# Kernel optimization log

Measured on AMD Instinct MI355X. Metric: run time of the kernel, lower is better.

Reference implementation:

```python
import jax, jax.numpy as jnp
import numpy as np

NEG_SLOPE = 0.2
N_GRAPHS = 32

def gat_conv(x, src, dst, W, attn_l, attn_r, bias):
    """DGL-style GATConv: returns [N, H, D]."""
    H, D = attn_l.shape
    N = x.shape[0]
    feat = (x @ W).reshape(N, H, D)                     # [N,H,D]
    el = jnp.sum(feat * attn_l[None], axis=-1)          # [N,H]
    er = jnp.sum(feat * attn_r[None], axis=-1)          # [N,H]
    e = jax.nn.leaky_relu(el[src] + er[dst], NEG_SLOPE) # [E,H]
    # edge softmax over incoming edges of each dst node
    emax = jax.ops.segment_max(e, dst, num_segments=N)
    emax = jnp.where(jnp.isfinite(emax), emax, 0.0)     # zero in-degree guard
    ex = jnp.exp(e - emax[dst])
    den = jax.ops.segment_sum(ex, dst, num_segments=N)
    alpha = ex / jnp.maximum(den[dst], 1e-9)            # [E,H]
    msg = alpha[:, :, None] * feat[src]                 # [E,H,D]
    rst = jax.ops.segment_sum(msg, dst, num_segments=N) # [N,H,D]
    return rst + bias.reshape(1, H, D)

def branch(x, src, dst, gid, W1, al1, ar1, b1, W2, al2, ar2, b2):
    h = jax.nn.relu(gat_conv(x, src, dst, W1, al1, ar1, b1))  # [N,10,64]
    h = h.sum(axis=1)                                          # [N,64]
    h = jax.nn.relu(gat_conv(h, src, dst, W2, al2, ar2, b2))  # [N,1,128]
    h = h[:, 0, :]                                             # [N,128]
    g = jax.ops.segment_max(h, gid, num_segments=N_GRAPHS)     # [B,128] max readout
    return jnp.where(jnp.isfinite(g), g, 0.0)

def reference(lig_x, lig_src, lig_dst, lig_gid, rec_x, rec_src, rec_dst, rec_gid,
              W1l, al1l, ar1l, b1l, W2l, al2l, ar2l, b2l,
              W1r, al1r, ar1r, b1r, W2r, al2r, ar2r, b2r,
              Wlin1, blin1, Wlin2, blin2):
    hlig = branch(lig_x, lig_src, lig_dst, lig_gid, W1l, al1l, ar1l, b1l, W2l, al2l, ar2l, b2l)
    hrec = branch(rec_x, rec_src, rec_dst, rec_gid, W1r, al1r, ar1r, b1r, W2r, al2r, ar2r, b2r)
    h = jnp.concatenate([hlig, hrec], axis=1)           # [B,256]
    h = jax.nn.relu(h @ Wlin1 + blin1)
    h = jax.nn.relu(h @ Wlin2 + blin2)
    return h.reshape(-1)

def setup_inputs() -> dict:
    key = jax.random.key(0)
    ks = jax.random.split(key, 24)
    Nl, El, Nr, Er = 20000, 160000, 40000, 400000
    d = {}
    d['lig_x'] = jax.random.normal(ks[0], (Nl, 64), jnp.float32)
    d['lig_src'] = jax.random.randint(ks[1], (El,), 0, Nl, jnp.int32)
    d['lig_dst'] = jax.random.randint(ks[2], (El,), 0, Nl, jnp.int32)
    d['lig_gid'] = jnp.sort(jax.random.randint(ks[3], (Nl,), 0, N_GRAPHS, jnp.int32))
    d['rec_x'] = jax.random.normal(ks[4], (Nr, 64), jnp.float32)
    d['rec_src'] = jax.random.randint(ks[5], (Er,), 0, Nr, jnp.int32)
    d['rec_dst'] = jax.random.randint(ks[6], (Er,), 0, Nr, jnp.int32)
    d['rec_gid'] = jnp.sort(jax.random.randint(ks[7], (Nr,), 0, N_GRAPHS, jnp.int32))
    s = 0.1
    d['W1l'] = jax.random.normal(ks[8], (64, 640), jnp.float32) * s
    d['al1l'] = jax.random.normal(ks[9], (10, 64), jnp.float32) * s
    d['ar1l'] = jax.random.normal(ks[10], (10, 64), jnp.float32) * s
    d['b1l'] = jnp.zeros((640,), jnp.float32)
    d['W2l'] = jax.random.normal(ks[11], (64, 128), jnp.float32) * s
    d['al2l'] = jax.random.normal(ks[12], (1, 128), jnp.float32) * s
    d['ar2l'] = jax.random.normal(ks[13], (1, 128), jnp.float32) * s
    d['b2l'] = jnp.zeros((128,), jnp.float32)
    d['W1r'] = jax.random.normal(ks[14], (64, 640), jnp.float32) * s
    d['al1r'] = jax.random.normal(ks[15], (10, 64), jnp.float32) * s
    d['ar1r'] = jax.random.normal(ks[16], (10, 64), jnp.float32) * s
    d['b1r'] = jnp.zeros((640,), jnp.float32)
    d['W2r'] = jax.random.normal(ks[17], (64, 128), jnp.float32) * s
    d['al2r'] = jax.random.normal(ks[18], (1, 128), jnp.float32) * s
    d['ar2r'] = jax.random.normal(ks[19], (1, 128), jnp.float32) * s
    d['b2r'] = jnp.zeros((128,), jnp.float32)
    d['Wlin1'] = jax.random.normal(ks[20], (256, 128), jnp.float32) * s
    d['blin1'] = jnp.zeros((128,), jnp.float32)
    d['Wlin2'] = jax.random.normal(ks[21], (128, 1), jnp.float32) * s
    d['blin2'] = jnp.zeros((1,), jnp.float32)
    return d
```

## Files before the change

### kernel.cpp

```cpp
#include <hip/hip_runtime.h>
#include <hip/hip_bf16.h>

typedef short bf16x8 __attribute__((ext_vector_type(8)));
typedef float f32x4 __attribute__((ext_vector_type(4)));

__device__ inline float lrelu(float x) { return x > 0.f ? x : 0.2f * x; }

__device__ inline unsigned short f2bf(float f) {
    unsigned u = __float_as_uint(f);
    u = u + 0x7FFFu + ((u >> 16) & 1u);
    return (unsigned short)(u >> 16);
}

__global__ void copy_x2(const float4* __restrict__ a, int na4,
                        const float4* __restrict__ b, int nb4, float4* __restrict__ o) {
    int total = na4 + nb4;
    int stride = gridDim.x * blockDim.x;
    for (int i = blockIdx.x * blockDim.x + threadIdx.x; i < total; i += stride)
        o[i] = (i < na4) ? a[i] : b[i - na4];
}

__global__ void fold_attn(const float* __restrict__ W, const float* __restrict__ al,
                          const float* __restrict__ ar, float* __restrict__ Walr,
                          int H, int D) {
    int k = blockIdx.x;
    int lane = threadIdx.x;
    int C = H * D;
    for (int h = 0; h < H; ++h) {
        float sl = 0.f, sr = 0.f;
        for (int d = lane; d < D; d += 64) {
            float w = W[(size_t)k * C + h * D + d];
            sl += w * al[h * D + d];
            sr += w * ar[h * D + d];
        }
        for (int off = 32; off; off >>= 1) {
            sl += __shfl_down(sl, off);
            sr += __shfl_down(sr, off);
        }
        if (lane == 0) {
            Walr[k * 2 * H + h] = sl;
            Walr[k * 2 * H + H + h] = sr;
        }
    }
}

__global__ void prep_walr(const float* __restrict__ Walr, unsigned short* __restrict__ F,
                          int C2) {
    int NCT = (C2 + 15) / 16;
    int total = NCT * 1024;
    int stride = gridDim.x * blockDim.x;
    for (int idx = blockIdx.x * blockDim.x + threadIdx.x; idx < total; idx += stride) {
        int j = idx & 7;
        int lane = (idx >> 3) & 63;
        int step = (idx >> 9) & 1;
        int CT = idx >> 10;
        int k = ((lane >> 4) << 3) + j + (step << 5);
        int col = (CT << 4) + (lane & 15);
        F[idx] = (col < C2) ? f2bf(Walr[k * C2 + col]) : 0;
    }
}

template <int H>
__global__ __launch_bounds__(256) void attn_mfma(const float* __restrict__ x,
                                                 const bf16x8* __restrict__ Wf,
                                                 float* __restrict__ el,
                                                 float* __restrict__ er, int N) {
    const int NCT = (2 * H + 15) / 16;
    int lane = threadIdx.x & 63;
    int w = threadIdx.x >> 6;
    int row0 = blockIdx.x * 64 + w * 16;
    int arow = row0 + (lane & 15);
    if (arow > N - 1) arow = N - 1;
    int kb = (lane >> 4) * 8;
    int colL = lane & 15;

    const float* xr = x + (size_t)arow * 64 + kb;
    float4 a0 = *reinterpret_cast<const float4*>(xr);
    float4 a1 = *reinterpret_cast<const float4*>(xr + 4);
    float4 a2 = *reinterpret_cast<const float4*>(xr + 32);
    float4 a3 = *reinterpret_cast<const float4*>(xr + 36);
    bf16x8 A0, A1;
    A0[0] = (short)f2bf(a0.x); A0[1] = (short)f2bf(a0.y);
    A0[2] = (short)f2bf(a0.z); A0[3] = (short)f2bf(a0.w);
    A0[4] = (short)f2bf(a1.x); A0[5] = (short)f2bf(a1.y);
    A0[6] = (short)f2bf(a1.z); A0[7] = (short)f2bf(a1.w);
    A1[0] = (short)f2bf(a2.x); A1[1] = (short)f2bf(a2.y);
    A1[2] = (short)f2bf(a2.z); A1[3] = (short)f2bf(a2.w);
    A1[4] = (short)f2bf(a3.x); A1[5] = (short)f2bf(a3.y);
    A1[6] = (short)f2bf(a3.z); A1[7] = (short)f2bf(a3.w);

    int rbase = row0 + (lane >> 4) * 4;
#pragma unroll
    for (int ct = 0; ct < NCT; ++ct) {
        bf16x8 B0 = Wf[(ct * 2 + 0) * 64 + lane];
        bf16x8 B1 = Wf[(ct * 2 + 1) * 64 + lane];
        f32x4 acc = {0, 0, 0, 0};
        acc = __builtin_amdgcn_mfma_f32_16x16x32_bf16(A0, B0, acc, 0, 0, 0);
        acc = __builtin_amdgcn_mfma_f32_16x16x32_bf16(A1, B1, acc, 0, 0, 0);
        int col = ct * 16 + colL;
#pragma unroll
        for (int r = 0; r < 4; ++r) {
            int row = rbase + r;
            if (row < N) {
                if (col < H) el[(size_t)row * H + col] = acc[r];
                else if (col < 2 * H) er[(size_t)row * H + col - H] = acc[r];
            }
        }
    }
}

__global__ void count_deg2(const int* __restrict__ dl, const int* __restrict__ dr,
                           int* __restrict__ deg, int El, int Er, int Nl) {
    int total = El + Er;
    int stride = gridDim.x * blockDim.x;
    for (int i = blockIdx.x * blockDim.x + threadIdx.x; i < total; i += stride) {
        int d = (i < El) ? dl[i] : (dr[i - El] + Nl);
        atomicAdd(&deg[d], 1);
    }
}

__global__ __launch_bounds__(256) void scan_local(const int* __restrict__ deg,
                                                  int* __restrict__ rowptr,
                                                  int* __restrict__ bsum, int N) {
    __shared__ int wsum[4];
    int t = threadIdx.x;
    int base = blockIdx.x * 2048 + t * 8;
    int v[8];
    int s = 0;
#pragma unroll
    for (int i = 0; i < 8; ++i) {
        int idx = base + i;
        v[i] = (idx < N) ? deg[idx] : 0;
        s += v[i];
    }
    int lane = t & 63, w = t >> 6;
    int incl = s;
    for (int off = 1; off < 64; off <<= 1) {
        int o = __shfl_up(incl, off);
        if (lane >= off) incl += o;
    }
    if (lane == 63) wsum[w] = incl;
    __syncthreads();
    int woff = 0;
    for (int i = 0; i < w; ++i) woff += wsum[i];
    int run = woff + incl - s;
#pragma unroll
    for (int i = 0; i < 8; ++i) {
        int idx = base + i;
        if (idx < N) rowptr[idx] = run;
        run += v[i];
    }
    if (t == 255) bsum[blockIdx.x] = woff + incl;
}

__global__ void scan_bsum(int* __restrict__ bsum, int* __restrict__ rowptrN, int nb) {
    int t = threadIdx.x;
    int v = (t < nb) ? bsum[t] : 0;
    int incl = v;
    for (int off = 1; off < 64; off <<= 1) {
        int o = __shfl_up(incl, off);
        if (t >= off) incl += o;
    }
    if (t < nb) bsum[t] = incl - v;
    if (t == 63) *rowptrN = incl;
}

__global__ __launch_bounds__(256) void scan_add(int* __restrict__ rowptr,
                                                const int* __restrict__ bsum, int N) {
    int off = bsum[blockIdx.x];
    if (off == 0) return;
    int base = blockIdx.x * 2048 + threadIdx.x * 8;
#pragma unroll
    for (int i = 0; i < 8; ++i) {
        int idx = base + i;
        if (idx < N) rowptr[idx] += off;
    }
}

__global__ void fill_adj2(const int* __restrict__ sl, const int* __restrict__ dl,
                          const int* __restrict__ sr, const int* __restrict__ dr,
                          int* __restrict__ cursor, int* __restrict__ adj,
                          int El, int Er, int Nl) {
    int total = El + Er;
    int stride = gridDim.x * blockDim.x;
    for (int i = blockIdx.x * blockDim.x + threadIdx.x; i < total; i += stride) {
        int s, d;
        if (i < El) { s = sl[i]; d = dl[i]; }
        else        { s = sr[i - El] + Nl; d = dr[i - El] + Nl; }
        int pos = atomicAdd(&cursor[d], 1);
        adj[pos] = s;
    }
}

__global__ __launch_bounds__(256) void dslot_expand(const int* __restrict__ rowptr,
                                                    int* __restrict__ dslot, int N) {
    int stride = gridDim.x * blockDim.x;
    for (int n = blockIdx.x * blockDim.x + threadIdx.x; n < N; n += stride) {
        int rb = rowptr[n], re = rowptr[n + 1];
        for (int j = rb; j < re; ++j) dslot[j] = n;
    }
}

__global__ void gstart_build2(const int* __restrict__ gidL, const int* __restrict__ gidR,
                              int* __restrict__ gs, int Nl, int Nr) {
    int Nc = Nl + Nr;
    int stride = gridDim.x * blockDim.x;
    for (int n = blockIdx.x * blockDim.x + threadIdx.x; n < Nc; n += stride) {
        if (n < Nl) {
            int gcur = gidL[n];
            int gprev = (n == 0) ? -1 : gidL[n - 1];
            for (int g = gprev + 1; g <= gcur; ++g) gs[g] = n;
            if (n == Nl - 1)
                for (int g = gcur + 1; g <= 32; ++g) gs[g] = Nl;
        } else {
            int ln = n - Nl;
            int gcur = gidR[ln];
            int gprev = (ln == 0) ? -1 : gidR[ln - 1];
            for (int g = gprev + 1; g <= gcur; ++g) gs[33 + g] = n;
            if (ln == Nr - 1)
                for (int g = gcur + 1; g <= 32; ++g) gs[33 + g] = Nc;
        }
    }
}

template <int H>
__global__ void edge_e(const int* __restrict__ adj, const int* __restrict__ dslot,
                       const float* __restrict__ el, const float* __restrict__ er,
                       float* __restrict__ e, int E) {
    int stride = gridDim.x * blockDim.x;
    for (int i = blockIdx.x * blockDim.x + threadIdx.x; i < E; i += stride) {
        int s = adj[i], d = dslot[i];
        const float* els = el + (size_t)s * H;
        const float* erd = er + (size_t)d * H;
#pragma unroll
        for (int h = 0; h < H; ++h)
            e[(size_t)i * H + h] = lrelu(els[h] + erd[h]);
    }
}

template <int H>
__global__ void node_norm(const int* __restrict__ rowptr, const float* __restrict__ e,
                          float* __restrict__ alpha, int N) {
    int stride = gridDim.x * blockDim.x;
    for (int n = blockIdx.x * blockDim.x + threadIdx.x; n < N; n += stride) {
        int rbeg = rowptr[n], rend = rowptr[n + 1];
        if (rbeg == rend) continue;
        float m[H], den[H];
#pragma unroll
        for (int h = 0; h < H; ++h) { m[h] = -INFINITY; den[h] = 0.f; }
        for (int j = rbeg; j < rend; ++j) {
#pragma unroll
            for (int h = 0; h < H; ++h) {
                float ev = e[(size_t)j * H + h];
                float newm = fmaxf(m[h], ev);
                den[h] = den[h] * __expf(m[h] - newm) + __expf(ev - newm);
                m[h] = newm;
            }
        }
        float inv[H];
#pragma unroll
        for (int h = 0; h < H; ++h) inv[h] = 1.f / fmaxf(den[h], 1e-9f);
        for (int j = rbeg; j < rend; ++j) {
#pragma unroll
            for (int h = 0; h < H; ++h)
                alpha[(size_t)j * H + h] = __expf(e[(size_t)j * H + h] - m[h]) * inv[h];
        }
    }
}

template <int H>
__global__ __launch_bounds__(256, 8) void gather_z_b(
        const int* __restrict__ rowptr, const int* __restrict__ adj,
        const float* __restrict__ alpha, const float* __restrict__ x,
        unsigned short* __restrict__ z, int N) {
    int lane = threadIdx.x & 63;
    int w = threadIdx.x >> 6;
    int wpb = blockDim.x >> 6;
    int wstride = gridDim.x * wpb;
    for (int n = blockIdx.x * wpb + w; n < N; n += wstride) {
        int rbeg = __builtin_amdgcn_readfirstlane(rowptr[n]);
        int rend = __builtin_amdgcn_readfirstlane(rowptr[n + 1]);
        float acc[H];
#pragma unroll
        for (int h = 0; h < H; ++h) acc[h] = 0.f;
        for (int base = rbeg; base < rend; base += 64) {
            int cnt = rend - base; if (cnt > 64) cnt = 64;
            int sv = adj[base + ((lane < cnt) ? lane : 0)];
            int j = 0;
            for (; j + 4 <= cnt; j += 4) {
                int s0 = __shfl(sv, j);
                int s1 = __shfl(sv, j + 1);
                int s2 = __shfl(sv, j + 2);
                int s3 = __shfl(sv, j + 3);
                float x0 = x[(size_t)s0 * 64 + lane];
                float x1 = x[(size_t)s1 * 64 + lane];
                float x2 = x[(size_t)s2 * 64 + lane];
                float x3 = x[(size_t)s3 * 64 + lane];
                const float* a0 = alpha + (size_t)(base + j) * H;
                const float* a1 = a0 + H;
                const float* a2 = a1 + H;
                const float* a3 = a2 + H;
#pragma unroll
                for (int h = 0; h < H; ++h)
                    acc[h] += a0[h] * x0 + a1[h] * x1 + a2[h] * x2 + a3[h] * x3;
            }
            for (; j < cnt; ++j) {
                int s = __shfl(sv, j);
                float xv = x[(size_t)s * 64 + lane];
                const float* al = alpha + (size_t)(base + j) * H;
#pragma unroll
                for (int h = 0; h < H; ++h) acc[h] += al[h] * xv;
            }
        }
#pragma unroll
        for (int h = 0; h < H; ++h)
            z[(size_t)n * (H * 64) + h * 64 + lane] = f2bf(acc[h]);
    }
}

__global__ void prep_wfrag(const float* __restrict__ W, unsigned short* __restrict__ F,
                           int C) {
    int total = (C >> 4) * 1024;
    int stride = gridDim.x * blockDim.x;
    for (int idx = blockIdx.x * blockDim.x + threadIdx.x; idx < total; idx += stride) {
        int j = idx & 7;
        int lane = (idx >> 3) & 63;
        int step = (idx >> 9) & 1;
        int CT = idx >> 10;
        int k = ((lane >> 4) << 3) + j + (step << 5);
        int col = (CT << 4) + (lane & 15);
        F[idx] = f2bf(W[(size_t)k * C + col]);
    }
}

template <int H>
__global__ __launch_bounds__(256) void gemm_heads_mfma_b(
        const unsigned short* __restrict__ z, const bf16x8* __restrict__ Wf,
        const float* __restrict__ bias, float* __restrict__ out, int N) {
    const int SA = H * 64;
    int lane = threadIdx.x & 63;
    int w = threadIdx.x >> 6;
    int row0 = blockIdx.x * 64 + w * 16;
    int arow = row0 + (lane & 15);
    if (arow > N - 1) arow = N - 1;
    int kb = (lane >> 4) * 8;
    int colL = lane & 15;

    f32x4 o0 = {0,0,0,0}, o1 = {0,0,0,0}, o2 = {0,0,0,0}, o3 = {0,0,0,0};

    for (int h = 0; h < H; ++h) {
        const unsigned short* zr = z + (size_t)arow * SA + h * 64 + kb;
        bf16x8 A0 = *reinterpret_cast<const bf16x8*>(zr);
        bf16x8 A1 = *reinterpret_cast<const bf16x8*>(zr + 32);

        f32x4 acc0 = {0,0,0,0}, acc1 = {0,0,0,0}, acc2 = {0,0,0,0}, acc3 = {0,0,0,0};
#define CT_STEP(accv, ct)                                                            \
        {                                                                            \
            bf16x8 B0 = Wf[((h * 4 + (ct)) * 2 + 0) * 64 + lane];                    \
            bf16x8 B1 = Wf[((h * 4 + (ct)) * 2 + 1) * 64 + lane];                    \
            accv = __builtin_amdgcn_mfma_f32_16x16x32_bf16(A0, B0, accv, 0, 0, 0);   \
            accv = __builtin_amdgcn_mfma_f32_16x16x32_bf16(A1, B1, accv, 0, 0, 0);   \
        }
        CT_STEP(acc0, 0) CT_STEP(acc1, 1) CT_STEP(acc2, 2) CT_STEP(acc3, 3)
#undef CT_STEP

#define EPI(ov, accv, ct)                                                            \
        {                                                                            \
            float bv = bias[h * 64 + (ct) * 16 + colL];                              \
            ov[0] += fmaxf(accv[0] + bv, 0.f);                                       \
            ov[1] += fmaxf(accv[1] + bv, 0.f);                                       \
            ov[2] += fmaxf(accv[2] + bv, 0.f);                                       \
            ov[3] += fmaxf(accv[3] + bv, 0.f);                                       \
        }
        EPI(o0, acc0, 0) EPI(o1, acc1, 1) EPI(o2, acc2, 2) EPI(o3, acc3, 3)
#undef EPI
    }

    int rbase = row0 + (lane >> 4) * 4;
#define ST(ov, ct)                                                                   \
    {                                                                                \
        _Pragma("unroll")                                                            \
        for (int r = 0; r < 4; ++r) {                                                \
            int row = rbase + r;                                                     \
            if (row < N) out[(size_t)row * 64 + (ct) * 16 + colL] = ov[r];           \
        }                                                                            \
    }
    ST(o0, 0) ST(o1, 1) ST(o2, 2) ST(o3, 3)
#undef ST
}

__global__ __launch_bounds__(256) void gemm_relu_mfma_b(
        const unsigned short* __restrict__ z, const bf16x8* __restrict__ Wf,
        const float* __restrict__ bias, float* __restrict__ out, int N) {
    int lane = threadIdx.x & 63;
    int w = threadIdx.x >> 6;
    int row0 = blockIdx.x * 64 + w * 16;
    int arow = row0 + (lane & 15);
    if (arow > N - 1) arow = N - 1;
    int kb = (lane >> 4) * 8;
    int colL = lane & 15;

    const unsigned short* zr = z + (size_t)arow * 64 + kb;
    bf16x8 A0 = *reinterpret_cast<const bf16x8*>(zr);
    bf16x8 A1 = *reinterpret_cast<const bf16x8*>(zr + 32);

    int rbase = row0 + (lane >> 4) * 4;
#define DO_CT(ct)                                                                    \
    {                                                                                \
        bf16x8 B0 = Wf[((ct) * 2 + 0) * 64 + lane];                                  \
        bf16x8 B1 = Wf[((ct) * 2 + 1) * 64 + lane];                                  \
        f32x4 acc = {0, 0, 0, 0};                                                    \
        acc = __builtin_amdgcn_mfma_f32_16x16x32_bf16(A0, B0, acc, 0, 0, 0);         \
        acc = __builtin_amdgcn_mfma_f32_16x16x32_bf16(A1, B1, acc, 0, 0, 0);         \
        float bv = bias[(ct) * 16 + colL];                                           \
        _Pragma("unroll")                                                            \
        for (int r = 0; r < 4; ++r) {                                                \
            int row = rbase + r;                                                     \
            if (row < N)                                                             \
                out[(size_t)row * 128 + (ct) * 16 + colL] = fmaxf(acc[r] + bv, 0.f); \
        }                                                                            \
    }
    DO_CT(0) DO_CT(1) DO_CT(2) DO_CT(3) DO_CT(4) DO_CT(5) DO_CT(6) DO_CT(7)
#undef DO_CT
}

__global__ __launch_bounds__(128) void graph_max2(const float* __restrict__ rst2,
                                                  const int* __restrict__ gstart,
                                                  float* __restrict__ gm) {
    int g = blockIdx.x;
    int b = g >> 5, gl = g & 31;
    int sp = blockIdx.y;
    int t = threadIdx.x;
    const int* gs = gstart + 33 * b;
    int rb = gs[gl], re = gs[gl + 1];
    float m = -INFINITY;
    for (int r = rb + sp; r < re; r += 8)
        m = fmaxf(m, rst2[(size_t)r * 128 + t]);
    gm[(size_t)((b * 8 + sp) * 32 + gl) * 128 + t] = m;
}

__global__ __launch_bounds__(256) void mlp_head2(
        const float* __restrict__ gml, const float* __restrict__ gmr,
        const float* __restrict__ W1, const float* __restrict__ b1,
        const float* __restrict__ W2, const float* __restrict__ b2,
        float* __restrict__ out) {
    __shared__ float hcat[256];
    __shared__ float part[256];
    __shared__ float h[128];
    int g = blockIdx.x;
    int t = threadIdx.x;
    {
        const float* gsrc = (t < 128) ? gml : gmr;
        int c = t & 127;
        float m = -INFINITY;
#pragma unroll
        for (int sp = 0; sp < 8; ++sp) m = fmaxf(m, gsrc[sp * 4096 + g * 128 + c]);
        hcat[t < 128 ? c : 128 + c] = fmaxf(m, 0.f);
    }
    __syncthreads();
    {
        int c = t & 127;
        int k0 = (t >> 7) << 7;
        float acc = 0.f;
#pragma unroll 4
        for (int k = 0; k < 128; ++k)
            acc += hcat[k0 + k] * W1[(size_t)(k0 + k) * 128 + c];
        part[t] = acc;
    }
    __syncthreads();
    if (t < 128) h[t] = fmaxf(part[t] + part[t + 128] + b1[t], 0.f);
    __syncthreads();
    if (t < 128) {
        float v = h[t] * W2[t];
        for (int off = 32; off; off >>= 1) v += __shfl_down(v, off);
        if ((t & 63) == 0) part[t >> 6] = v;
    }
    __syncthreads();
    if (t == 0) out[g] = fmaxf(part[0] + part[1] + b2[0], 0.f);
}

static inline unsigned nblk_elem(long long total) {
    long long b = (total + 255) / 256;
    if (b > 65535) b = 65535;
    if (b < 1) b = 1;
    return (unsigned)b;
}
static inline unsigned nblk_gather(long long nodes) {
    long long b = (nodes + 3) / 4;
    if (b > 65535) b = 65535;
    if (b < 1) b = 1;
    return (unsigned)b;
}

extern "C" void kernel_launch(void* const* d_in, const int* in_sizes, int n_in,
                              void* d_out, int out_size, void* d_ws, size_t ws_size,
                              hipStream_t stream) {
    const float* lig_x = (const float*)d_in[0];
    const int* lig_src = (const int*)d_in[1];
    const int* lig_dst = (const int*)d_in[2];
    const int* lig_gid = (const int*)d_in[3];
    const float* rec_x = (const float*)d_in[4];
    const int* rec_src = (const int*)d_in[5];
    const int* rec_dst = (const int*)d_in[6];
    const int* rec_gid = (const int*)d_in[7];
    const float* W1l = (const float*)d_in[8];
    const float* al1l = (const float*)d_in[9];
    const float* ar1l = (const float*)d_in[10];
    const float* b1l = (const float*)d_in[11];
    const float* W2l = (const float*)d_in[12];
    const float* al2l = (const float*)d_in[13];
    const float* ar2l = (const float*)d_in[14];
    const float* b2l = (const float*)d_in[15];
    const float* W1r = (const float*)d_in[16];
    const float* al1r = (const float*)d_in[17];
    const float* ar1r = (const float*)d_in[18];
    const float* b1r = (const float*)d_in[19];
    const float* W2r = (const float*)d_in[20];
    const float* al2r = (const float*)d_in[21];
    const float* ar2r = (const float*)d_in[22];
    const float* b2r = (const float*)d_in[23];
    const float* Wlin1 = (const float*)d_in[24];
    const float* blin1 = (const float*)d_in[25];
    const float* Wlin2 = (const float*)d_in[26];
    const float* blin2 = (const float*)d_in[27];

    int Nl = in_sizes[0] / 64, El = in_sizes[1];
    int Nr = in_sizes[4] / 64, Er = in_sizes[5];
    int Nc = Nl + Nr;
    int Ec = El + Er;

    char* ws = (char*)d_ws;
    float* xcat = (float*)ws;        ws += (size_t)Nc * 64 * 4;
    unsigned short* zb = (unsigned short*)ws;   ws += (size_t)Nc * 640 * 2;
    unsigned short* z2b = (unsigned short*)ws;  ws += (size_t)Nc * 64 * 2;
    float* h1 = (float*)ws;          ws += (size_t)Nc * 64 * 4;
    float* rst2 = (float*)ws;        ws += (size_t)Nc * 128 * 4;
    float* elb = (float*)ws;         ws += (size_t)Nc * 10 * 4;
    float* erb = (float*)ws;         ws += (size_t)Nc * 10 * 4;
    int* deg = (int*)ws;             ws += (size_t)Nc * 4;
    int* cursor = (int*)ws;          ws += (size_t)Nc * 4;
    int* rowptr = (int*)ws;          ws += (size_t)(Nc + 1) * 4;
    int* adj = (int*)ws;             ws += (size_t)Ec * 4;
    int* dslot = (int*)ws;           ws += (size_t)Ec * 4;
    float* ebuf = (float*)ws;        ws += (size_t)Ec * 10 * 4;
    float* alpha = (float*)ws;       ws += (size_t)Ec * 10 * 4;
    float* gm = (float*)ws;          ws += 2 * 8 * 32 * 128 * 4;
    int* gstart = (int*)ws;          ws += 66 * 4;
    int* bsum = (int*)ws;            ws += 64 * 4;
    float* walr1l = (float*)ws;      ws += 64 * 20 * 4;
    float* walr1r = (float*)ws;      ws += 64 * 20 * 4;
    float* walr2l = (float*)ws;      ws += 64 * 2 * 4;
    float* walr2r = (float*)ws;      ws += 64 * 2 * 4;
    unsigned short* wf1l = (unsigned short*)ws;  ws += 40960 * 2;
    unsigned short* wf1r = (unsigned short*)ws;  ws += 40960 * 2;
    unsigned short* wf2l = (unsigned short*)ws;  ws += 8192 * 2;
    unsigned short* wf2r = (unsigned short*)ws;  ws += 8192 * 2;
    unsigned short* wfa1l = (unsigned short*)ws; ws += 2048 * 2;
    unsigned short* wfa1r = (unsigned short*)ws; ws += 2048 * 2;
    unsigned short* wfa2l = (unsigned short*)ws; ws += 1024 * 2;
    unsigned short* wfa2r = (unsigned short*)ws; ws += 1024 * 2;

    int nb = (Nc + 2047) / 2048;

    prep_wfrag<<<40, 256, 0, stream>>>(W1l, wf1l, 640);
    prep_wfrag<<<40, 256, 0, stream>>>(W1r, wf1r, 640);
    prep_wfrag<<<8, 256, 0, stream>>>(W2l, wf2l, 128);
    prep_wfrag<<<8, 256, 0, stream>>>(W2r, wf2r, 128);
    fold_attn<<<64, 64, 0, stream>>>(W1l, al1l, ar1l, walr1l, 10, 64);
    fold_attn<<<64, 64, 0, stream>>>(W1r, al1r, ar1r, walr1r, 10, 64);
    fold_attn<<<64, 64, 0, stream>>>(W2l, al2l, ar2l, walr2l, 1, 128);
    fold_attn<<<64, 64, 0, stream>>>(W2r, al2r, ar2r, walr2r, 1, 128);
    prep_walr<<<8, 256, 0, stream>>>(walr1l, wfa1l, 20);
    prep_walr<<<8, 256, 0, stream>>>(walr1r, wfa1r, 20);
    prep_walr<<<4, 256, 0, stream>>>(walr2l, wfa2l, 2);
    prep_walr<<<4, 256, 0, stream>>>(walr2r, wfa2r, 2);

    copy_x2<<<nblk_elem((long long)Nc * 16), 256, 0, stream>>>(
        (const float4*)lig_x, Nl * 16, (const float4*)rec_x, Nr * 16, (float4*)xcat);
    hipMemsetAsync(deg, 0, (size_t)Nc * 4, stream);
    count_deg2<<<nblk_elem(Ec), 256, 0, stream>>>(lig_dst, rec_dst, deg, El, Er, Nl);
    scan_local<<<nb, 256, 0, stream>>>(deg, rowptr, bsum, Nc);
    scan_bsum<<<1, 64, 0, stream>>>(bsum, rowptr + Nc, nb);
    scan_add<<<nb, 256, 0, stream>>>(rowptr, bsum, Nc);
    hipMemcpyAsync(cursor, rowptr, (size_t)Nc * 4, hipMemcpyDeviceToDevice, stream);
    fill_adj2<<<nblk_elem(Ec), 256, 0, stream>>>(lig_src, lig_dst, rec_src, rec_dst,
                                                 cursor, adj, El, Er, Nl);
    dslot_expand<<<nblk_elem(Nc), 256, 0, stream>>>(rowptr, dslot, Nc);
    gstart_build2<<<nblk_elem(Nc), 256, 0, stream>>>(lig_gid, rec_gid, gstart, Nl, Nr);

    attn_mfma<10><<<(Nl + 63) / 64, 256, 0, stream>>>(xcat, (const bf16x8*)wfa1l,
                                                      elb, erb, Nl);
    attn_mfma<10><<<(Nr + 63) / 64, 256, 0, stream>>>(xcat + (size_t)Nl * 64,
                                                      (const bf16x8*)wfa1r,
                                                      elb + (size_t)Nl * 10,
                                                      erb + (size_t)Nl * 10, Nr);
    edge_e<10><<<nblk_elem(Ec), 256, 0, stream>>>(adj, dslot, elb, erb, ebuf, Ec);
    node_norm<10><<<nblk_elem(Nc), 256, 0, stream>>>(rowptr, ebuf, alpha, Nc);
    gather_z_b<10><<<nblk_gather(Nc), 256, 0, stream>>>(rowptr, adj, alpha, xcat, zb, Nc);
    gemm_heads_mfma_b<10><<<(Nl + 63) / 64, 256, 0, stream>>>(zb, (const bf16x8*)wf1l,
                                                              b1l, h1, Nl);
    gemm_heads_mfma_b<10><<<(Nr + 63) / 64, 256, 0, stream>>>(zb + (size_t)Nl * 640,
                                                              (const bf16x8*)wf1r, b1r,
                                                              h1 + (size_t)Nl * 64, Nr);

    attn_mfma<1><<<(Nl + 63) / 64, 256, 0, stream>>>(h1, (const bf16x8*)wfa2l,
                                                     elb, erb, Nl);
    attn_mfma<1><<<(Nr + 63) / 64, 256, 0, stream>>>(h1 + (size_t)Nl * 64,
                                                     (const bf16x8*)wfa2r,
                                                     elb + Nl, erb + Nl, Nr);
    edge_e<1><<<nblk_elem(Ec), 256, 0, stream>>>(adj, dslot, elb, erb, ebuf, Ec);
    node_norm<1><<<nblk_elem(Nc), 256, 0, stream>>>(rowptr, ebuf, alpha, Nc);
    gather_z_b<1><<<nblk_gather(Nc), 256, 0, stream>>>(rowptr, adj, alpha, h1, z2b, Nc);
    gemm_relu_mfma_b<<<(Nl + 63) / 64, 256, 0, stream>>>(z2b, (const bf16x8*)wf2l,
                                                         b2l, rst2, Nl);
    gemm_relu_mfma_b<<<(Nr + 63) / 64, 256, 0, stream>>>(z2b + (size_t)Nl * 64,
                                                         (const bf16x8*)wf2r, b2r,
                                                         rst2 + (size_t)Nl * 128, Nr);
    graph_max2<<<dim3(64, 8), 128, 0, stream>>>(rst2, gstart, gm);
    mlp_head2<<<32, 256, 0, stream>>>(gm, gm + 8 * 32 * 128, Wlin1, blin1, Wlin2, blin2,
                                      (float*)d_out);
}
```

Baseline: 351.9 us.

## Merge per-branch and setup kernels to cut launch count

Batches the ligand and receptor launches of the weight-prep, attention, and GEMM kernels into single launches that pick weights and row ranges by block index. Folds the x copy, degree zeroing and graph-start build into one init kernel. Fuses the scan offset add with the cursor copy and dslot expansion. The aim is to remove roughly fifteen small launches and a memcpy/memset from a latency-bound pipeline. The cost is some per-block branching and a serial dslot fill inside the scan-add threads.

```diff
diff --git a/kernel.cpp b/kernel.cpp
--- a/kernel.cpp
+++ b/kernel.cpp
@@ -12,17 +12,52 @@
     return (unsigned short)(u >> 16);
 }
 
-__global__ void copy_x2(const float4* __restrict__ a, int na4,
-                        const float4* __restrict__ b, int nb4, float4* __restrict__ o) {
-    int total = na4 + nb4;
+__global__ void init_misc(const float4* __restrict__ xl, int nl4,
+                          const float4* __restrict__ xr, int nr4,
+                          float4* __restrict__ xcat, int* __restrict__ deg,
+                          const int* __restrict__ gidL, const int* __restrict__ gidR,
+                          int* __restrict__ gs, int Nl, int Nr) {
+    int Nc = Nl + Nr;
     int stride = gridDim.x * blockDim.x;
-    for (int i = blockIdx.x * blockDim.x + threadIdx.x; i < total; i += stride)
-        o[i] = (i < na4) ? a[i] : b[i - na4];
-}
-
-__global__ void fold_attn(const float* __restrict__ W, const float* __restrict__ al,
-                          const float* __restrict__ ar, float* __restrict__ Walr,
-                          int H, int D) {
+    int tid = blockIdx.x * blockDim.x + threadIdx.x;
+    for (int i = tid; i < nl4 + nr4; i += stride)
+        xcat[i] = (i < nl4) ? xl[i] : xr[i - nl4];
+    for (int i = tid; i < Nc; i += stride) deg[i] = 0;
+    for (int n = tid; n < Nc; n += stride) {
+        if (n < Nl) {
+            int gcur = gidL[n];
+            int gprev = (n == 0) ? -1 : gidL[n - 1];
+            for (int g = gprev + 1; g <= gcur; ++g) gs[g] = n;
+            if (n == Nl - 1)
+                for (int g = gcur + 1; g <= 32; ++g) gs[g] = Nl;
+        } else {
+            int ln = n - Nl;
+            int gcur = gidR[ln];
+            int gprev = (ln == 0) ? -1 : gidR[ln - 1];
+            for (int g = gprev + 1; g <= gcur; ++g) gs[33 + g] = n;
+            if (ln == Nr - 1)
+                for (int g = gcur + 1; g <= 32; ++g) gs[33 + g] = Nc;
+        }
+    }
+}
+
+__global__ void fold_all(const float* __restrict__ W1l, const float* __restrict__ al1l,
+                         const float* __restrict__ ar1l, float* __restrict__ o1l,
+                         const float* __restrict__ W1r, const float* __restrict__ al1r,
+                         const float* __restrict__ ar1r, float* __restrict__ o1r,
+                         const float* __restrict__ W2l, const float* __restrict__ al2l,
+                         const float* __restrict__ ar2l, float* __restrict__ o2l,
+                         const float* __restrict__ W2r, const float* __restrict__ al2r,
+                         const float* __restrict__ ar2r, float* __restrict__ o2r) {
+    const float *W, *al, *ar;
+    float* o;
+    int H, D;
+    switch (blockIdx.y) {
+        case 0: W = W1l; al = al1l; ar = ar1l; o = o1l; H = 10; D = 64; break;
+        case 1: W = W1r; al = al1r; ar = ar1r; o = o1r; H = 10; D = 64; break;
+        case 2: W = W2l; al = al2l; ar = ar2l; o = o2l; H = 1; D = 128; break;
+        default: W = W2r; al = al2r; ar = ar2r; o = o2r; H = 1; D = 128; break;
+    }
     int k = blockIdx.x;
     int lane = threadIdx.x;
     int C = H * D;
@@ -38,18 +73,25 @@
             sr += __shfl_down(sr, off);
         }
         if (lane == 0) {
-            Walr[k * 2 * H + h] = sl;
-            Walr[k * 2 * H + H + h] = sr;
-        }
-    }
-}
-
-__global__ void prep_walr(const float* __restrict__ Walr, unsigned short* __restrict__ F,
-                          int C2) {
-    int NCT = (C2 + 15) / 16;
-    int total = NCT * 1024;
+            o[k * 2 * H + h] = sl;
+            o[k * 2 * H + H + h] = sr;
+        }
+    }
+}
+
+__global__ void prep_walr_all(const float* __restrict__ w1l, const float* __restrict__ w1r,
+                              const float* __restrict__ w2l, const float* __restrict__ w2r,
+                              unsigned short* __restrict__ f1l, unsigned short* __restrict__ f1r,
+                              unsigned short* __restrict__ f2l, unsigned short* __restrict__ f2r) {
     int stride = gridDim.x * blockDim.x;
-    for (int idx = blockIdx.x * blockDim.x + threadIdx.x; idx < total; idx += stride) {
+    for (int idx0 = blockIdx.x * blockDim.x + threadIdx.x; idx0 < 6144; idx0 += stride) {
+        const float* Walr;
+        unsigned short* F;
+        int C2, idx;
+        if (idx0 < 2048)      { Walr = w1l; F = f1l; C2 = 20; idx = idx0; }
+        else if (idx0 < 4096) { Walr = w1r; F = f1r; C2 = 20; idx = idx0 - 2048; }
+        else if (idx0 < 5120) { Walr = w2l; F = f2l; C2 = 2;  idx = idx0 - 4096; }
+        else                  { Walr = w2r; F = f2r; C2 = 2;  idx = idx0 - 5120; }
         int j = idx & 7;
         int lane = (idx >> 3) & 63;
         int step = (idx >> 9) & 1;
@@ -60,17 +102,46 @@
     }
 }
 
+__global__ void wfrag_all(const float* __restrict__ W1l, const float* __restrict__ W1r,
+                          const float* __restrict__ W2l, const float* __restrict__ W2r,
+                          unsigned short* __restrict__ f1l, unsigned short* __restrict__ f1r,
+                          unsigned short* __restrict__ f2l, unsigned short* __restrict__ f2r) {
+    int stride = gridDim.x * blockDim.x;
+    for (int idx0 = blockIdx.x * blockDim.x + threadIdx.x; idx0 < 98304; idx0 += stride) {
+        const float* W;
+        unsigned short* F;
+        int C, idx;
+        if (idx0 < 40960)      { W = W1l; F = f1l; C = 640; idx = idx0; }
+        else if (idx0 < 81920) { W = W1r; F = f1r; C = 640; idx = idx0 - 40960; }
+        else if (idx0 < 90112) { W = W2l; F = f2l; C = 128; idx = idx0 - 81920; }
+        else                   { W = W2r; F = f2r; C = 128; idx = idx0 - 90112; }
+        int j = idx & 7;
+        int lane = (idx >> 3) & 63;
+        int step = (idx >> 9) & 1;
+        int CT = idx >> 10;
+        int k = ((lane >> 4) << 3) + j + (step << 5);
+        int col = (CT << 4) + (lane & 15);
+        F[idx] = f2bf(W[(size_t)k * C + col]);
+    }
+}
+
 template <int H>
-__global__ __launch_bounds__(256) void attn_mfma(const float* __restrict__ x,
-                                                 const bf16x8* __restrict__ Wf,
-                                                 float* __restrict__ el,
-                                                 float* __restrict__ er, int N) {
+__global__ __launch_bounds__(256) void attn_mfma2(const float* __restrict__ x,
+                                                  const bf16x8* __restrict__ Wfl,
+                                                  const bf16x8* __restrict__ Wfr,
+                                                  float* __restrict__ el,
+                                                  float* __restrict__ er,
+                                                  int Nl, int Nc, int nbl) {
     const int NCT = (2 * H + 15) / 16;
     int lane = threadIdx.x & 63;
     int w = threadIdx.x >> 6;
-    int row0 = blockIdx.x * 64 + w * 16;
+    int b = blockIdx.x;
+    const bf16x8* Wf;
+    int row0, rend_;
+    if (b < nbl) { Wf = Wfl; row0 = b * 64 + w * 16; rend_ = Nl; }
+    else         { Wf = Wfr; row0 = Nl + (b - nbl) * 64 + w * 16; rend_ = Nc; }
     int arow = row0 + (lane & 15);
-    if (arow > N - 1) arow = N - 1;
+    if (arow > rend_ - 1) arow = rend_ - 1;
     int kb = (lane >> 4) * 8;
     int colL = lane & 15;
 
@@ -101,7 +172,7 @@
 #pragma unroll
         for (int r = 0; r < 4; ++r) {
             int row = rbase + r;
-            if (row < N) {
+            if (row < rend_) {
                 if (col < H) el[(size_t)row * H + col] = acc[r];
                 else if (col < 2 * H) er[(size_t)row * H + col - H] = acc[r];
             }
@@ -165,15 +236,23 @@
     if (t == 63) *rowptrN = incl;
 }
 
-__global__ __launch_bounds__(256) void scan_add(int* __restrict__ rowptr,
-                                                const int* __restrict__ bsum, int N) {
+__global__ __launch_bounds__(256) void scan_add_fused(int* __restrict__ rowptr,
+                                                      const int* __restrict__ bsum,
+                                                      const int* __restrict__ deg,
+                                                      int* __restrict__ cursor,
+                                                      int* __restrict__ dslot, int N) {
     int off = bsum[blockIdx.x];
-    if (off == 0) return;
     int base = blockIdx.x * 2048 + threadIdx.x * 8;
 #pragma unroll
     for (int i = 0; i < 8; ++i) {
         int idx = base + i;
-        if (idx < N) rowptr[idx] += off;
+        if (idx < N) {
+            int rp = rowptr[idx] + off;
+            rowptr[idx] = rp;
+            cursor[idx] = rp;
+            int dg = deg[idx];
+            for (int j = rp; j < rp + dg; ++j) dslot[j] = idx;
+        }
     }
 }
 
@@ -189,37 +268,6 @@
         else        { s = sr[i - El] + Nl; d = dr[i - El] + Nl; }
         int pos = atomicAdd(&cursor[d], 1);
         adj[pos] = s;
-    }
-}
-
-__global__ __launch_bounds__(256) void dslot_expand(const int* __restrict__ rowptr,
-                                                    int* __restrict__ dslot, int N) {
-    int stride = gridDim.x * blockDim.x;
-    for (int n = blockIdx.x * blockDim.x + threadIdx.x; n < N; n += stride) {
-        int rb = rowptr[n], re = rowptr[n + 1];
-        for (int j = rb; j < re; ++j) dslot[j] = n;
-    }
-}
-
-__global__ void gstart_build2(const int* __restrict__ gidL, const int* __restrict__ gidR,
-                              int* __restrict__ gs, int Nl, int Nr) {
-    int Nc = Nl + Nr;
-    int stride = gridDim.x * blockDim.x;
-    for (int n = blockIdx.x * blockDim.x + threadIdx.x; n < Nc; n += stride) {
-        if (n < Nl) {
-            int gcur = gidL[n];
-            int gprev = (n == 0) ? -1 : gidL[n - 1];
-            for (int g = gprev + 1; g <= gcur; ++g) gs[g] = n;
-            if (n == Nl - 1)
-                for (int g = gcur + 1; g <= 32; ++g) gs[g] = Nl;
-        } else {
-            int ln = n - Nl;
-            int gcur = gidR[ln];
-            int gprev = (ln == 0) ? -1 : gidR[ln - 1];
-            for (int g = gprev + 1; g <= gcur; ++g) gs[33 + g] = n;
-            if (ln == Nr - 1)
-                for (int g = gcur + 1; g <= 32; ++g) gs[33 + g] = Nc;
-        }
     }
 }
 
@@ -318,31 +366,23 @@
     }
 }
 
-__global__ void prep_wfrag(const float* __restrict__ W, unsigned short* __restrict__ F,
-                           int C) {
-    int total = (C >> 4) * 1024;
-    int stride = gridDim.x * blockDim.x;
-    for (int idx = blockIdx.x * blockDim.x + threadIdx.x; idx < total; idx += stride) {
-        int j = idx & 7;
-        int lane = (idx >> 3) & 63;
-        int step = (idx >> 9) & 1;
-        int CT = idx >> 10;
-        int k = ((lane >> 4) << 3) + j + (step << 5);
-        int col = (CT << 4) + (lane & 15);
-        F[idx] = f2bf(W[(size_t)k * C + col]);
-    }
-}
-
 template <int H>
-__global__ __launch_bounds__(256) void gemm_heads_mfma_b(
-        const unsigned short* __restrict__ z, const bf16x8* __restrict__ Wf,
-        const float* __restrict__ bias, float* __restrict__ out, int N) {
+__global__ __launch_bounds__(256) void gemm_heads2(
+        const unsigned short* __restrict__ z, const bf16x8* __restrict__ Wfl,
+        const bf16x8* __restrict__ Wfr, const float* __restrict__ bl,
+        const float* __restrict__ br, float* __restrict__ out,
+        int Nl, int Nc, int nbl) {
     const int SA = H * 64;
     int lane = threadIdx.x & 63;
     int w = threadIdx.x >> 6;
-    int row0 = blockIdx.x * 64 + w * 16;
+    int b = blockIdx.x;
+    const bf16x8* Wf;
+    const float* bias;
+    int row0, rend_;
+    if (b < nbl) { Wf = Wfl; bias = bl; row0 = b * 64 + w * 16; rend_ = Nl; }
+    else         { Wf = Wfr; bias = br; row0 = Nl + (b - nbl) * 64 + w * 16; rend_ = Nc; }
     int arow = row0 + (lane & 15);
-    if (arow > N - 1) arow = N - 1;
+    if (arow > rend_ - 1) arow = rend_ - 1;
     int kb = (lane >> 4) * 8;
     int colL = lane & 15;
 
@@ -382,21 +422,28 @@
         _Pragma("unroll")                                                            \
         for (int r = 0; r < 4; ++r) {                                                \
             int row = rbase + r;                                                     \
-            if (row < N) out[(size_t)row * 64 + (ct) * 16 + colL] = ov[r];           \
+            if (row < rend_) out[(size_t)row * 64 + (ct) * 16 + colL] = ov[r];       \
         }                                                                            \
     }
     ST(o0, 0) ST(o1, 1) ST(o2, 2) ST(o3, 3)
 #undef ST
 }
 
-__global__ __launch_bounds__(256) void gemm_relu_mfma_b(
-        const unsigned short* __restrict__ z, const bf16x8* __restrict__ Wf,
-        const float* __restrict__ bias, float* __restrict__ out, int N) {
+__global__ __launch_bounds__(256) void gemm_relu2(
+        const unsigned short* __restrict__ z, const bf16x8* __restrict__ Wfl,
+        const bf16x8* __restrict__ Wfr, const float* __restrict__ bl,
+        const float* __restrict__ br, float* __restrict__ out,
+        int Nl, int Nc, int nbl) {
     int lane = threadIdx.x & 63;
     int w = threadIdx.x >> 6;
-    int row0 = blockIdx.x * 64 + w * 16;
+    int b = blockIdx.x;
+    const bf16x8* Wf;
+    const float* bias;
+    int row0, rend_;
+    if (b < nbl) { Wf = Wfl; bias = bl; row0 = b * 64 + w * 16; rend_ = Nl; }
+    else         { Wf = Wfr; bias = br; row0 = Nl + (b - nbl) * 64 + w * 16; rend_ = Nc; }
     int arow = row0 + (lane & 15);
-    if (arow > N - 1) arow = N - 1;
+    if (arow > rend_ - 1) arow = rend_ - 1;
     int kb = (lane >> 4) * 8;
     int colL = lane & 15;
 
@@ -416,7 +463,7 @@
         _Pragma("unroll")                                                            \
         for (int r = 0; r < 4; ++r) {                                                \
             int row = rbase + r;                                                     \
-            if (row < N)                                                             \
+            if (row < rend_)                                                         \
                 out[(size_t)row * 128 + (ct) * 16 + colL] = fmaxf(acc[r] + bv, 0.f); \
         }                                                                            \
     }
@@ -528,6 +575,8 @@
     int Nr = in_sizes[4] / 64, Er = in_sizes[5];
     int Nc = Nl + Nr;
     int Ec = El + Er;
+    int nbl = (Nl + 63) / 64;
+    int nbr = (Nr + 63) / 64;
 
     char* ws = (char*)d_ws;
     float* xcat = (float*)ws;        ws += (size_t)Nc * 64 * 4;
@@ -562,60 +611,43 @@
 
     int nb = (Nc + 2047) / 2048;
 
-    prep_wfrag<<<40, 256, 0, stream>>>(W1l, wf1l, 640);
-    prep_wfrag<<<40, 256, 0, stream>>>(W1r, wf1r, 640);
-    prep_wfrag<<<8, 256, 0, stream>>>(W2l, wf2l, 128);
-    prep_wfrag<<<8, 256, 0, stream>>>(W2r, wf2r, 128);
-    fold_attn<<<64, 64, 0, stream>>>(W1l, al1l, ar1l, walr1l, 10, 64);
-    fold_attn<<<64, 64, 0, stream>>>(W1r, al1r, ar1r, walr1r, 10, 64);
-    fold_attn<<<64, 64, 0, stream>>>(W2l, al2l, ar2l, walr2l, 1, 128);
-    fold_attn<<<64, 64, 0, stream>>>(W2r, al2r, ar2r, walr2r, 1, 128);
-    prep_walr<<<8, 256, 0, stream>>>(walr1l, wfa1l, 20);
-    prep_walr<<<8, 256, 0, stream>>>(walr1r, wfa1r, 20);
-    prep_walr<<<4, 256, 0, stream>>>(walr2l, wfa2l, 2);
-    prep_walr<<<4, 256, 0, stream>>>(walr2r, wfa2r, 2);
-
-    copy_x2<<<nblk_elem((long long)Nc * 16), 256, 0, stream>>>(
-        (const float4*)lig_x, Nl * 16, (const float4*)rec_x, Nr * 16, (float4*)xcat);
-    hipMemsetAsync(deg, 0, (size_t)Nc * 4, stream);
+    wfrag_all<<<96, 256, 0, stream>>>(W1l, W1r, W2l, W2r, wf1l, wf1r, wf2l, wf2r);
+    fold_all<<<dim3(64, 4), 64, 0, stream>>>(W1l, al1l, ar1l, walr1l,
+                                             W1r, al1r, ar1r, walr1r,
+                                             W2l, al2l, ar2l, walr2l,
+                                             W2r, al2r, ar2r, walr2r);
+    prep_walr_all<<<24, 256, 0, stream>>>(walr1l, walr1r, walr2l, walr2r,
+                                          wfa1l, wfa1r, wfa2l, wfa2r);
+
+    init_misc<<<nblk_elem((long long)Nc * 16), 256, 0, stream>>>(
+        (const float4*)lig_x, Nl * 16, (const float4*)rec_x, Nr * 16, (float4*)xcat,
+        deg, lig_gid, rec_gid, gstart, Nl, Nr);
     count_deg2<<<nblk_elem(Ec), 256, 0, stream>>>(lig_dst, rec_dst, deg, El, Er, Nl);
     scan_local<<<nb, 256, 0, stream>>>(deg, rowptr, bsum, Nc);
     scan_bsum<<<1, 64, 0, stream>>>(bsum, rowptr + Nc, nb);
-    scan_add<<<nb, 256, 0, stream>>>(rowptr, bsum, Nc);
-    hipMemcpyAsync(cursor, rowptr, (size_t)Nc * 4, hipMemcpyDeviceToDevice, stream);
+    scan_add_fused<<<nb, 256, 0, stream>>>(rowptr, bsum, deg, cursor, dslot, Nc);
     fill_adj2<<<nblk_elem(Ec), 256, 0, stream>>>(lig_src, lig_dst, rec_src, rec_dst,
                                                  cursor, adj, El, Er, Nl);
-    dslot_expand<<<nblk_elem(Nc), 256, 0, stream>>>(rowptr, dslot, Nc);
-    gstart_build2<<<nblk_elem(Nc), 256, 0, stream>>>(lig_gid, rec_gid, gstart, Nl, Nr);
-
-    attn_mfma<10><<<(Nl + 63) / 64, 256, 0, stream>>>(xcat, (const bf16x8*)wfa1l,
-                                                      elb, erb, Nl);
-    attn_mfma<10><<<(Nr + 63) / 64, 256, 0, stream>>>(xcat + (size_t)Nl * 64,
-                                                      (const bf16x8*)wfa1r,
-                                                      elb + (size_t)Nl * 10,
-                                                      erb + (size_t)Nl * 10, Nr);
+
+    attn_mfma2<10><<<nbl + nbr, 256, 0, stream>>>(xcat, (const bf16x8*)wfa1l,
+                                                  (const bf16x8*)wfa1r, elb, erb,
+                                                  Nl, Nc, nbl);
     edge_e<10><<<nblk_elem(Ec), 256, 0, stream>>>(adj, dslot, elb, erb, ebuf, Ec);
     node_norm<10><<<nblk_elem(Nc), 256, 0, stream>>>(rowptr, ebuf, alpha, Nc);
     gather_z_b<10><<<nblk_gather(Nc), 256, 0, stream>>>(rowptr, adj, alpha, xcat, zb, Nc);
-    gemm_heads_mfma_b<10><<<(Nl + 63) / 64, 256, 0, stream>>>(zb, (const bf16x8*)wf1l,
-                                                              b1l, h1, Nl);
-    gemm_heads_mfma_b<10><<<(Nr + 63) / 64, 256, 0, stream>>>(zb + (size_t)Nl * 640,
-                                                              (const bf16x8*)wf1r, b1r,
-                                                              h1 + (size_t)Nl * 64, Nr);
-
-    attn_mfma<1><<<(Nl + 63) / 64, 256, 0, stream>>>(h1, (const bf16x8*)wfa2l,
-                                                     elb, erb, Nl);
-    attn_mfma<1><<<(Nr + 63) / 64, 256, 0, stream>>>(h1 + (size_t)Nl * 64,
-                                                     (const bf16x8*)wfa2r,
-                                                     elb + Nl, erb + Nl, Nr);
+    gemm_heads2<10><<<nbl + nbr, 256, 0, stream>>>(zb, (const bf16x8*)wf1l,
+                                                   (const bf16x8*)wf1r, b1l, b1r,
+                                                   h1, Nl, Nc, nbl);
+
+    attn_mfma2<1><<<nbl + nbr, 256, 0, stream>>>(h1, (const bf16x8*)wfa2l,
+                                                 (const bf16x8*)wfa2r, elb, erb,
+                                                 Nl, Nc, nbl);
     edge_e<1><<<nblk_elem(Ec), 256, 0, stream>>>(adj, dslot, elb, erb, ebuf, Ec);
     node_norm<1><<<nblk_elem(Nc), 256, 0, stream>>>(rowptr, ebuf, alpha, Nc);
     gather_z_b<1><<<nblk_gather(Nc), 256, 0, stream>>>(rowptr, adj, alpha, h1, z2b, Nc);
-    gemm_relu_mfma_b<<<(Nl + 63) / 64, 256, 0, stream>>>(z2b, (const bf16x8*)wf2l,
-                                                         b2l, rst2, Nl);
-    gemm_relu_mfma_b<<<(Nr + 63) / 64, 256, 0, stream>>>(z2b + (size_t)Nl * 64,
-                                                         (const bf16x8*)wf2r, b2r,
-                                                         rst2 + (size_t)Nl * 128, Nr);
+    gemm_relu2<<<nbl + nbr, 256, 0, stream>>>(z2b, (const bf16x8*)wf2l,
+                                              (const bf16x8*)wf2r, b2l, b2r,
+                                              rst2, Nl, Nc, nbl);
     graph_max2<<<dim3(64, 8), 128, 0, stream>>>(rst2, gstart, gm);
     mlp_head2<<<32, 256, 0, stream>>>(gm, gm + 8 * 32 * 128, Wlin1, blin1, Wlin2, blin2,
                                       (float*)d_out);
```

Measured after the change: 302.3 us, median of 2. 14.1% less time.
